# Optimization experiments

Hardware: AMD Instinct MI355X
Metric: run time of the kernel (lower is better)

## Reference

```python
import jax, jax.numpy as jnp
import numpy as np

N = 50000   # nodes
E = 640000  # edges
IN = 128    # input feature dim (== H*C so every layer has a residual)
H = 4       # heads
C = 32      # out channels per head
L = 3       # layers
D = H * C   # 128, per-layer output width
NEG_SLOPE = 0.2
LN_EPS = 1e-5


def setup_inputs() -> dict:
    key = jax.random.key(0)
    ks = jax.random.split(key, 6)
    s = 0.1  # keep activations well-scaled
    x = jax.random.normal(ks[0], (N, IN), dtype=jnp.float32)
    edge_index = jax.random.randint(ks[1], (2, E), 0, N)
    Wl = jax.random.normal(ks[2], (L, IN, D), dtype=jnp.float32) * s
    bl = jnp.zeros((L, D), dtype=jnp.float32)
    Wr = jax.random.normal(ks[3], (L, IN, D), dtype=jnp.float32) * s
    br = jnp.zeros((L, D), dtype=jnp.float32)
    att = jax.random.normal(ks[4], (L, H, C), dtype=jnp.float32) * s
    bias = jnp.zeros((L, D), dtype=jnp.float32)
    gamma = jnp.ones((L, D), dtype=jnp.float32)
    beta = jnp.zeros((L, D), dtype=jnp.float32)
    return {"x": x, "edge_index": edge_index, "Wl": Wl, "bl": bl,
            "Wr": Wr, "br": br, "att": att, "bias": bias,
            "gamma": gamma, "beta": beta}


def _gatv2_layer(x, src, dst, Wl, bl, Wr, br, att, bias):
    # GATv2Conv (concat heads, eval mode so attention dropout is identity)
    xl = (x @ Wl + bl).reshape(N, H, C)  # source transform
    xr = (x @ Wr + br).reshape(N, H, C)  # target transform
    # edge-wise gather: message along edge j->i uses xl[j] + xr[i]
    e = jax.nn.leaky_relu(xl[src] + xr[dst], NEG_SLOPE)      # [E,H,C]
    logit = jnp.einsum('ehc,hc->eh', e, att)                  # [E,H]
    # segment softmax over incoming edges of each target node
    m = jax.ops.segment_max(logit, dst, num_segments=N)       # [N,H]
    a = jnp.exp(logit - m[dst])
    denom = jax.ops.segment_sum(a, dst, num_segments=N)       # [N,H]
    a = a / (denom[dst] + 1e-16)
    # scatter-aggregate weighted source messages
    out = jax.ops.segment_sum(a[:, :, None] * xl[src], dst, num_segments=N)
    return out.reshape(N, D) + bias


def _layer_norm(h, g, b):
    mu = jnp.mean(h, axis=-1, keepdims=True)
    var = jnp.mean((h - mu) ** 2, axis=-1, keepdims=True)
    return (h - mu) * jax.lax.rsqrt(var + LN_EPS) * g + b


def reference(x, edge_index, Wl, bl, Wr, br, att, bias, gamma, beta):
    src, dst = edge_index[0], edge_index[1]
    out = x
    for l in range(L):  # small fixed layer count
        h = jax.nn.relu(_gatv2_layer(out, src, dst, Wl[l], bl[l], Wr[l], br[l], att[l], bias[l]))
        h = _layer_norm(h, gamma[l], beta[l])
        out = h + out  # in_dim == hidden*heads, so residual at every layer
    return out
```

## Files before the change

kernel.cpp:

```cpp
#include <hip/hip_runtime.h>
#include <hip/hip_bf16.h>
#include <math.h>

#define N_NODES 50000
#define N_EDGES 640000
#define DIM 128
#define NLAYER 3
#define LN_EPS 1e-5f
#define LOG2E 1.44269504088896f
#define NSCAN 49

#if __has_builtin(__builtin_amdgcn_exp2f)
#define EXP2(x) __builtin_amdgcn_exp2f(x)
#else
#define EXP2(x) exp2f(x)
#endif

typedef __attribute__((ext_vector_type(8))) short bf16x8;
typedef __attribute__((ext_vector_type(4))) float f32x4;

__device__ inline ushort f2b(float f) {
    __hip_bfloat16 h = __float2bfloat16(f);
    return *reinterpret_cast<ushort*>(&h);
}
__device__ inline float bf_lo(unsigned u) { return __uint_as_float(u << 16); }
__device__ inline float bf_hi(unsigned u) { return __uint_as_float(u & 0xffff0000u); }
__device__ inline float lr(float t) { return fmaf(0.4f, fabsf(t), 0.6f * t); }
__device__ inline unsigned pack2(float a, float b) {
    return (unsigned)f2b(a) | ((unsigned)f2b(b) << 16);
}
__device__ inline int cw_of(int w) { return (w & 15) + 32 * (w >> 4); }

template<int CTRL>
__device__ inline float dppadd(float v) {
    int m = __builtin_amdgcn_update_dpp(0, __float_as_int(v), CTRL, 0xF, 0xF, true);
    return v + __int_as_float(m);
}
__device__ inline float reduce16(float v) {
    v = dppadd<0x124>(v);
    v = dppadd<0x128>(v);
    v = dppadd<0xB1>(v);
    v = dppadd<0x4E>(v);
    return v;
}


__global__ __launch_bounds__(256) void fusedinit(
    const float* __restrict__ x, unsigned* __restrict__ curb,
    const float* __restrict__ Wl, const float* __restrict__ Wr, ushort* __restrict__ Wt,
    const int* __restrict__ dst, int* __restrict__ deg,
    const float* __restrict__ att, const float* __restrict__ bias,
    const float* __restrict__ gamma, const float* __restrict__ beta,
    float2* __restrict__ params)
{
    int b = blockIdx.x, t = threadIdx.x;
    if (b < 12500) {
        int i = b * 256 + t;
        int node = i >> 6, w = i & 63;
        int c = cw_of(w);
        curb[i] = pack2(x[node * DIM + c], x[node * DIM + c + 16]);
    } else if (b < 12884) {
        int i = (b - 12500) * 256 + t;
        if (i < NLAYER * 2 * DIM * DIM) {
            int p = i & 127, n = (i >> 7) & 127, mat = (i >> 14) & 1, l = i >> 15;
            int c = cw_of(p >> 1) + (p & 1) * 16;
            const float* W = mat ? Wr : Wl;
            Wt[i] = f2b(W[l * DIM * DIM + c * DIM + n]);
        }
    } else if (b < 15384) {
        int e = (b - 12884) * 256 + t;
        atomicAdd(&deg[dst[e]], 1);
    } else {
        int i = t;
        if (i < NLAYER * 64) {
            int l = i >> 6, w = i & 63;
            int c = cw_of(w);
            const float* A = att + l * DIM;
            const float* B = bias + l * DIM;
            const float* G = gamma + l * DIM;
            const float* E = beta + l * DIM;
            params[l * 256 + w]       = make_float2(A[c] * LOG2E, A[c + 16] * LOG2E);
            params[l * 256 + 64 + w]  = make_float2(B[c], B[c + 16]);
            params[l * 256 + 128 + w] = make_float2(G[c], G[c + 16]);
            params[l * 256 + 192 + w] = make_float2(E[c], E[c + 16]);
        }
    }
}


__global__ __launch_bounds__(1024) void scan1(const int* __restrict__ deg,
                                              int* __restrict__ rowptr,
                                              int* __restrict__ bsum,
                                              int* __restrict__ blockhist) {
    __shared__ int sd[1024];
    __shared__ int lh[256];
    int t = threadIdx.x;
    int idx = blockIdx.x * 1024 + t;
    if (t < 256) lh[t] = 0;
    __syncthreads();
    int v = (idx < N_NODES) ? deg[idx] : 0;
    if (idx < N_NODES) atomicAdd(&lh[v < 255 ? v : 255], 1);
    sd[t] = v;
    __syncthreads();
    for (int off = 1; off < 1024; off <<= 1) {
        int add = (t >= off) ? sd[t - off] : 0;
        __syncthreads();
        sd[t] += add;
        __syncthreads();
    }
    if (idx < N_NODES) rowptr[idx + 1] = sd[t];
    if (t == 1023) bsum[blockIdx.x] = sd[1023];
    if (t < 256) blockhist[blockIdx.x * 256 + t] = lh[t];
}

__global__ __launch_bounds__(1024) void midscan(const int* __restrict__ bsum,
                                                int* __restrict__ bcarry,
                                                const int* __restrict__ blockhist,
                                                int* __restrict__ bboff) {
    __shared__ int sh[256];
    int t = threadIdx.x;
    if (t < 256) {
        int tot = 0;
        for (int b = 0; b < NSCAN; ++b) tot += blockhist[b * 256 + t];
        sh[t] = tot;
    }
    __syncthreads();
    for (int off = 1; off < 256; off <<= 1) {
        int add = 0;
        if (t < 256 && t >= off) add = sh[t - off];
        __syncthreads();
        if (t < 256) sh[t] += add;
        __syncthreads();
    }
    if (t < 256) {
        int run = sh[255] - sh[t];
        for (int b = 0; b < NSCAN; ++b) {
            bboff[b * 256 + t] = run;
            run += blockhist[b * 256 + t];
        }
    }
    if (t == 0) {
        int c = 0;
        for (int b = 0; b < NSCAN; ++b) { bcarry[b] = c; c += bsum[b]; }
    }
}

__global__ __launch_bounds__(1024) void scan2(int* __restrict__ rowptr,
                                              const int* __restrict__ bcarry,
                                              const int* __restrict__ deg,
                                              const int* __restrict__ bboff,
                                              int* __restrict__ order) {
    __shared__ int lh[256];
    int t = threadIdx.x;
    int idx = blockIdx.x * 1024 + t;
    if (t < 256) lh[t] = 0;
    __syncthreads();
    int carry = bcarry[blockIdx.x];
    if (idx == 0) rowptr[0] = 0;
    if (idx < N_NODES) {
        rowptr[idx + 1] += carry;
        int d = deg[idx];
        int bin = d < 255 ? d : 255;
        int rank = atomicAdd(&lh[bin], 1);
        order[bboff[blockIdx.x * 256 + bin] + rank] = idx;
    }
}

__global__ void scatter_kernel(const int* __restrict__ src, const int* __restrict__ dst,
                               const int* __restrict__ rowptr, int* __restrict__ cnt,
                               int* __restrict__ esrc) {
    int e = blockIdx.x * blockDim.x + threadIdx.x;
    if (e < N_EDGES) {
        int d = dst[e];
        int pos = rowptr[d] + atomicAdd(&cnt[d], 1);
        esrc[pos] = src[e] << 8;
    }
}


__global__ __launch_bounds__(256) void gemm_mfma(
    const ushort* __restrict__ A,
    const ushort* __restrict__ Wt_l,
    const float* __restrict__ bl, const float* __restrict__ br,
    unsigned* __restrict__ xlb, unsigned* __restrict__ xrb)
{
    int mat = blockIdx.y;
    int rowbase = blockIdx.x * 128;
    int wid = threadIdx.x >> 6;
    int lane = threadIdx.x & 63;
    int wr = wid >> 1, wc = wid & 1;
    int m0 = rowbase + wr * 64, n0 = wc * 64;

    const ushort* W = Wt_l + mat * DIM * DIM;
    const float* bias = mat ? br : bl;
    unsigned* out = mat ? xrb : xlb;

    int fr = lane & 15;
    int kg = lane >> 4;

    bf16x8 af[4][4], bfr[4][4];
    #pragma unroll
    for (int mf = 0; mf < 4; ++mf) {
        int row = m0 + mf * 16 + fr;
        if (row > N_NODES - 1) row = N_NODES - 1;
        const ushort* p = A + (size_t)row * DIM + kg * 8;
        #pragma unroll
        for (int kf = 0; kf < 4; ++kf)
            af[mf][kf] = *reinterpret_cast<const bf16x8*>(p + kf * 32);
    }
    #pragma unroll
    for (int nf = 0; nf < 4; ++nf) {
        const ushort* p = W + (size_t)(n0 + nf * 16 + fr) * DIM + kg * 8;
        #pragma unroll
        for (int kf = 0; kf < 4; ++kf)
            bfr[nf][kf] = *reinterpret_cast<const bf16x8*>(p + kf * 32);
    }

    f32x4 acc[4][4];
    #pragma unroll
    for (int mf = 0; mf < 4; ++mf)
        #pragma unroll
        for (int nf = 0; nf < 4; ++nf)
            acc[mf][nf] = (f32x4){0.f, 0.f, 0.f, 0.f};

    #pragma unroll
    for (int kf = 0; kf < 4; ++kf)
        #pragma unroll
        for (int mf = 0; mf < 4; ++mf)
            #pragma unroll
            for (int nf = 0; nf < 4; ++nf)
                acc[mf][nf] = __builtin_amdgcn_mfma_f32_16x16x32_bf16(
                    af[mf][kf], bfr[nf][kf], acc[mf][nf], 0, 0, 0);

    int col = lane & 15;
    int r4 = lane >> 4;
    float bb[4];
    #pragma unroll
    for (int nf = 0; nf < 4; ++nf) bb[nf] = bias[n0 + nf * 16 + col];

    #pragma unroll
    for (int mf = 0; mf < 4; ++mf) {
        #pragma unroll
        for (int pj = 0; pj < 2; ++pj) {
            int w = col + 32 * wc + 16 * pj;
            #pragma unroll
            for (int r = 0; r < 4; ++r) {
                int row = m0 + mf * 16 + r4 * 4 + r;
                if (row < N_NODES)
                    out[(size_t)row * 64 + w] =
                        pack2(acc[mf][2 * pj][r] + bb[2 * pj],
                              acc[mf][2 * pj + 1][r] + bb[2 * pj + 1]);
            }
        }
    }
}


template<int U>
__device__ inline void edge_batch(const char* __restrict__ xb,
                                  const int* __restrict__ esrc, int e, int laneoff,
                                  float ax, float ay, float xrx, float xry,
                                  float& s, float& ox, float& oy) {
    int j[U]; unsigned u[U]; float vx[U], vy[U], p[U];
    #pragma unroll
    for (int i = 0; i < U; ++i) j[i] = esrc[e + i];
    #pragma unroll
    for (int i = 0; i < U; ++i)
        u[i] = *(const unsigned*)(xb + j[i] + laneoff);
    #pragma unroll
    for (int i = 0; i < U; ++i) {
        vx[i] = bf_lo(u[i]); vy[i] = bf_hi(u[i]);
        p[i] = lr(vx[i] + xrx) * ax + lr(vy[i] + xry) * ay;
    }
    #pragma unroll
    for (int i = 0; i < U; ++i) p[i] = reduce16(p[i]);
    #pragma unroll
    for (int i = 0; i < U; ++i) {
        float w = EXP2(p[i]);
        s += w; ox = fmaf(w, vx[i], ox); oy = fmaf(w, vy[i], oy);
    }
}

__global__ __launch_bounds__(256) void agg_kernel(
    const unsigned* __restrict__ xlb2, const unsigned* __restrict__ xrb2,
    const int* __restrict__ esrc, const int* __restrict__ rowptr,
    const int* __restrict__ order, const float2* __restrict__ P4,
    unsigned* __restrict__ curb, float* __restrict__ outf, int last)
{
    int slot = blockIdx.x * 4 + (threadIdx.x >> 6);
    int lane = threadIdx.x & 63;
    if (slot >= N_NODES) return;
    int node = __builtin_amdgcn_readfirstlane(order[slot]);

    unsigned xru = xrb2[node * 64 + lane];
    float xrx = bf_lo(xru), xry = bf_hi(xru);
    float2 att2 = P4[lane];

    const char* xb = (const char*)xlb2;
    int laneoff = lane << 2;

    float s = 0.f, ox = 0.f, oy = 0.f;
    int e0 = rowptr[node], e1 = rowptr[node + 1];

    int e = e0;
    for (; e + 8 <= e1; e += 8)
        edge_batch<8>(xb, esrc, e, laneoff, att2.x, att2.y, xrx, xry, s, ox, oy);
    if (e + 4 <= e1) {
        edge_batch<4>(xb, esrc, e, laneoff, att2.x, att2.y, xrx, xry, s, ox, oy);
        e += 4;
    }
    for (; e < e1; ++e)
        edge_batch<1>(xb, esrc, e, laneoff, att2.x, att2.y, xrx, xry, s, ox, oy);

    float inv = 1.f / (s + 1e-16f);
    float2 b2 = P4[64 + lane];
    float gx = fmaxf(fmaf(ox, inv, b2.x), 0.f);
    float gy = fmaxf(fmaf(oy, inv, b2.y), 0.f);

    float sum = gx + gy;
    sum = reduce16(sum);
    sum += __shfl_xor(sum, 16);
    sum += __shfl_xor(sum, 32);
    float mu = sum * (1.f / 128.f);
    float dx = gx - mu, dy = gy - mu;
    float ss = dx * dx + dy * dy;
    ss = reduce16(ss);
    ss += __shfl_xor(ss, 16);
    ss += __shfl_xor(ss, 32);
    float rstd = rsqrtf(ss * (1.f / 128.f) + LN_EPS);

    float2 g2  = P4[128 + lane];
    float2 be2 = P4[192 + lane];
    unsigned old = curb[node * 64 + lane];
    float yx = fmaf(dx * rstd, g2.x, be2.x) + bf_lo(old);
    float yy = fmaf(dy * rstd, g2.y, be2.y) + bf_hi(old);

    if (last) {
        int c = cw_of(lane);
        outf[node * DIM + c] = yx;
        outf[node * DIM + c + 16] = yy;
    } else {
        curb[node * 64 + lane] = pack2(yx, yy);
    }
}


extern "C" void kernel_launch(void* const* d_in, const int* in_sizes, int n_in,
                              void* d_out, int out_size, void* d_ws, size_t ws_size,
                              hipStream_t stream) {
    const float* x     = (const float*)d_in[0];
    const int*   ei    = (const int*)d_in[1];
    const float* Wl    = (const float*)d_in[2];
    const float* bl    = (const float*)d_in[3];
    const float* Wr    = (const float*)d_in[4];
    const float* br    = (const float*)d_in[5];
    const float* att   = (const float*)d_in[6];
    const float* bias  = (const float*)d_in[7];
    const float* gamma = (const float*)d_in[8];
    const float* beta  = (const float*)d_in[9];
    float* outf = (float*)d_out;

    char* ws = (char*)d_ws;
    size_t off = 0;
    auto alloc = [&](size_t bytes) -> void* {
        void* p = ws + off;
        off += (bytes + 255) & ~size_t(255);
        return p;
    };
    unsigned* curb = (unsigned*)alloc((size_t)N_NODES * 64 * 4);
    unsigned* xlb  = (unsigned*)alloc((size_t)N_NODES * 64 * 4);
    unsigned* xrb  = (unsigned*)alloc((size_t)N_NODES * 64 * 4);
    ushort* Wt     = (ushort*)alloc((size_t)NLAYER * 2 * DIM * DIM * 2);
    int* esrc      = (int*)alloc((size_t)N_EDGES * 4);
    int* rowptr    = (int*)alloc((size_t)(N_NODES + 1) * 4);
    int* zbase     = (int*)alloc((size_t)(2 * N_NODES + 2 * 64) * 4);
    int* deg = zbase, *cnt = zbase + N_NODES;
    int* bsum = cnt + N_NODES, *bcarry = bsum + 64;
    int* blockhist = (int*)alloc((size_t)NSCAN * 256 * 4);
    int* bboff     = (int*)alloc((size_t)NSCAN * 256 * 4);
    int* order     = (int*)alloc((size_t)N_NODES * 4);
    float2* params = (float2*)alloc((size_t)NLAYER * 256 * sizeof(float2));

    const int* srcArr = ei;
    const int* dstArr = ei + N_EDGES;

    hipMemsetAsync(zbase, 0, (size_t)(2 * N_NODES + 2 * 64) * 4, stream);
    fusedinit<<<15385, 256, 0, stream>>>(x, curb, Wl, Wr, Wt, dstArr, deg,
                                         att, bias, gamma, beta, params);
    scan1<<<NSCAN, 1024, 0, stream>>>(deg, rowptr, bsum, blockhist);
    midscan<<<1, 1024, 0, stream>>>(bsum, bcarry, blockhist, bboff);
    scan2<<<NSCAN, 1024, 0, stream>>>(rowptr, bcarry, deg, bboff, order);
    scatter_kernel<<<(N_EDGES + 255) / 256, 256, 0, stream>>>(srcArr, dstArr, rowptr, cnt, esrc);

    for (int l = 0; l < NLAYER; ++l) {
        gemm_mfma<<<dim3((N_NODES + 127) / 128, 2), 256, 0, stream>>>(
            (const ushort*)curb, Wt + (size_t)l * 2 * DIM * DIM,
            bl + (size_t)l * DIM, br + (size_t)l * DIM, xlb, xrb);
        agg_kernel<<<(N_NODES + 3) / 4, 256, 0, stream>>>(
            xlb, xrb, esrc, rowptr, order, params + (size_t)l * 256,
            curb, outf, l == NLAYER - 1 ? 1 : 0);
    }
}
```

Measured before the change: 261.5 us.

## Software-pipeline edge gathers in aggregation and replace memset with zero kernel

The aggregation loop now prefetches the next batch of eight source indices and feature gathers while computing the current batch, using a double-buffered register scheme. The tail is handled by a masked eight-wide gather with clamped indices instead of separate 4- and 1-wide paths. The aim is to hide gather latency behind the attention math. It also replaces hipMemsetAsync with a small zero-fill kernel to cut launch overhead. The extra in-flight registers may lower occupancy.

```diff
diff --git a/kernel.cpp b/kernel.cpp
--- a/kernel.cpp
+++ b/kernel.cpp
@@ -42,6 +42,12 @@
     v = dppadd<0xB1>(v);
     v = dppadd<0x4E>(v);
     return v;
+}
+
+
+__global__ __launch_bounds__(256) void zerofill(int4* __restrict__ p, int n4) {
+    int i = blockIdx.x * 256 + threadIdx.x;
+    if (i < n4) p[i] = make_int4(0, 0, 0, 0);
 }
 
 
@@ -256,28 +262,38 @@
 }
 
 
-template<int U>
-__device__ inline void edge_batch(const char* __restrict__ xb,
-                                  const int* __restrict__ esrc, int e, int laneoff,
-                                  float ax, float ay, float xrx, float xry,
-                                  float& s, float& ox, float& oy) {
-    int j[U]; unsigned u[U]; float vx[U], vy[U], p[U];
-    #pragma unroll
-    for (int i = 0; i < U; ++i) j[i] = esrc[e + i];
-    #pragma unroll
-    for (int i = 0; i < U; ++i)
+__device__ inline void gather8(const char* __restrict__ xb, int laneoff,
+                               const int j[8], unsigned u[8]) {
+    #pragma unroll
+    for (int i = 0; i < 8; ++i)
         u[i] = *(const unsigned*)(xb + j[i] + laneoff);
-    #pragma unroll
-    for (int i = 0; i < U; ++i) {
-        vx[i] = bf_lo(u[i]); vy[i] = bf_hi(u[i]);
-        p[i] = lr(vx[i] + xrx) * ax + lr(vy[i] + xry) * ay;
-    }
-    #pragma unroll
-    for (int i = 0; i < U; ++i) p[i] = reduce16(p[i]);
-    #pragma unroll
-    for (int i = 0; i < U; ++i) {
-        float w = EXP2(p[i]);
-        s += w; ox = fmaf(w, vx[i], ox); oy = fmaf(w, vy[i], oy);
+}
+
+__device__ inline void compute8(const unsigned u[8], float ax, float ay,
+                                float xrx, float xry,
+                                float& s, float& ox, float& oy) {
+    #pragma unroll
+    for (int i = 0; i < 8; ++i) {
+        float vx = bf_lo(u[i]), vy = bf_hi(u[i]);
+        float p = lr(vx + xrx) * ax + lr(vy + xry) * ay;
+        p = reduce16(p);
+        float w = EXP2(p);
+        s += w; ox = fmaf(w, vx, ox); oy = fmaf(w, vy, oy);
+    }
+}
+
+__device__ inline void computeT(const unsigned u[8], float ax, float ay,
+                                float xrx, float xry,
+                                float& s, float& ox, float& oy, int rem) {
+    #pragma unroll
+    for (int i = 0; i < 8; ++i) {
+        if (i < rem) {
+            float vx = bf_lo(u[i]), vy = bf_hi(u[i]);
+            float p = lr(vx + xrx) * ax + lr(vy + xry) * ay;
+            p = reduce16(p);
+            float w = EXP2(p);
+            s += w; ox = fmaf(w, vx, ox); oy = fmaf(w, vy, oy);
+        }
     }
 }
 
@@ -301,16 +317,47 @@
 
     float s = 0.f, ox = 0.f, oy = 0.f;
     int e0 = rowptr[node], e1 = rowptr[node + 1];
-
-    int e = e0;
-    for (; e + 8 <= e1; e += 8)
-        edge_batch<8>(xb, esrc, e, laneoff, att2.x, att2.y, xrx, xry, s, ox, oy);
-    if (e + 4 <= e1) {
-        edge_batch<4>(xb, esrc, e, laneoff, att2.x, att2.y, xrx, xry, s, ox, oy);
-        e += 4;
-    }
-    for (; e < e1; ++e)
-        edge_batch<1>(xb, esrc, e, laneoff, att2.x, att2.y, xrx, xry, s, ox, oy);
+    int nb = (e1 - e0) >> 3;
+    int rem = (e1 - e0) & 7;
+
+    int jc[8], jn[8];
+    unsigned uc[8], un[8];
+
+    if (nb > 0) {
+        #pragma unroll
+        for (int i = 0; i < 8; ++i) jc[i] = esrc[e0 + i];
+        gather8(xb, laneoff, jc, uc);
+    }
+    int ec = e0;
+    for (int b = 1; b < nb; ++b) {
+        int en = ec + 8;
+        #pragma unroll
+        for (int i = 0; i < 8; ++i) jn[i] = esrc[en + i];
+        gather8(xb, laneoff, jn, un);
+        compute8(uc, att2.x, att2.y, xrx, xry, s, ox, oy);
+        #pragma unroll
+        for (int i = 0; i < 8; ++i) uc[i] = un[i];
+        ec = en;
+    }
+    if (nb > 0) {
+        if (rem) {
+            int et = ec + 8;
+            #pragma unroll
+            for (int i = 0; i < 8; ++i)
+                jn[i] = esrc[et + (i < rem ? i : rem - 1)];
+            gather8(xb, laneoff, jn, un);
+            compute8(uc, att2.x, att2.y, xrx, xry, s, ox, oy);
+            computeT(un, att2.x, att2.y, xrx, xry, s, ox, oy, rem);
+        } else {
+            compute8(uc, att2.x, att2.y, xrx, xry, s, ox, oy);
+        }
+    } else if (rem) {
+        #pragma unroll
+        for (int i = 0; i < 8; ++i)
+            jc[i] = esrc[e0 + (i < rem ? i : rem - 1)];
+        gather8(xb, laneoff, jc, uc);
+        computeT(uc, att2.x, att2.y, xrx, xry, s, ox, oy, rem);
+    }
 
     float inv = 1.f / (s + 1e-16f);
     float2 b2 = P4[64 + lane];
@@ -384,7 +431,8 @@
     const int* srcArr = ei;
     const int* dstArr = ei + N_EDGES;
 
-    hipMemsetAsync(zbase, 0, (size_t)(2 * N_NODES + 2 * 64) * 4, stream);
+    int n4 = (2 * N_NODES + 2 * 64) / 4;
+    zerofill<<<(n4 + 255) / 256, 256, 0, stream>>>((int4*)zbase, n4);
     fusedinit<<<15385, 256, 0, stream>>>(x, curb, Wl, Wr, Wt, dstArr, deg,
                                          att, bias, gamma, beta, params);
     scan1<<<NSCAN, 1024, 0, stream>>>(deg, rowptr, bsum, blockhist);
```

Measured after the change: 257.7 us. About the same (-1.5%).

## Split aggregation per head with head-major layout and padded 4-edge CSR rows

Applied to the files above, without the earlier changes.

Stores xl/xr head-major, so each head's 32 channels sit in a contiguous 64-byte row. Aggregation is split into a per-head kernel, where each wave handles one head of one node and processes four edges at once (16 lanes each) from 4-aligned padded CSR rows, plus a separate LayerNorm/residual kernel. The goal is smaller gathered rows, better cache locality per head, and more edge-level parallelism. In exchange it adds an extra kernel, a bf16 round-trip for the aggregated output, padding waste on short rows, and a custom zero-fill kernel in place of memset.

```diff
diff --git a/kernel.cpp b/kernel.cpp
--- a/kernel.cpp
+++ b/kernel.cpp
@@ -4,6 +4,7 @@
 
 #define N_NODES 50000
 #define N_EDGES 640000
+#define EPAD (N_EDGES + 4 * N_NODES)
 #define DIM 128
 #define NLAYER 3
 #define LN_EPS 1e-5f
@@ -42,6 +43,12 @@
     v = dppadd<0xB1>(v);
     v = dppadd<0x4E>(v);
     return v;
+}
+
+
+__global__ __launch_bounds__(256) void zerofill(int4* __restrict__ p, int n4) {
+    int i = blockIdx.x * 256 + threadIdx.x;
+    if (i < n4) p[i] = make_int4(0, 0, 0, 0);
 }
 
 
@@ -100,7 +107,7 @@
     __syncthreads();
     int v = (idx < N_NODES) ? deg[idx] : 0;
     if (idx < N_NODES) atomicAdd(&lh[v < 255 ? v : 255], 1);
-    sd[t] = v;
+    sd[t] = (v + 3) & ~3;
     __syncthreads();
     for (int off = 1; off < 1024; off <<= 1) {
         int add = (t >= off) ? sd[t - off] : 0;
@@ -173,7 +180,7 @@
     if (e < N_EDGES) {
         int d = dst[e];
         int pos = rowptr[d] + atomicAdd(&cnt[d], 1);
-        esrc[pos] = src[e] << 8;
+        esrc[pos] = src[e] << 6;
     }
 }
 
@@ -182,7 +189,7 @@
     const ushort* __restrict__ A,
     const ushort* __restrict__ Wt_l,
     const float* __restrict__ bl, const float* __restrict__ br,
-    unsigned* __restrict__ xlb, unsigned* __restrict__ xrb)
+    unsigned* __restrict__ xlh, unsigned* __restrict__ xrh)
 {
     int mat = blockIdx.y;
     int rowbase = blockIdx.x * 128;
@@ -193,7 +200,7 @@
 
     const ushort* W = Wt_l + mat * DIM * DIM;
     const float* bias = mat ? br : bl;
-    unsigned* out = mat ? xrb : xlb;
+    unsigned* out = mat ? xrh : xlh;
 
     int fr = lane & 15;
     int kg = lane >> 4;
@@ -242,12 +249,12 @@
     for (int mf = 0; mf < 4; ++mf) {
         #pragma unroll
         for (int pj = 0; pj < 2; ++pj) {
-            int w = col + 32 * wc + 16 * pj;
+            int h = 2 * wc + pj;
             #pragma unroll
             for (int r = 0; r < 4; ++r) {
                 int row = m0 + mf * 16 + r4 * 4 + r;
                 if (row < N_NODES)
-                    out[(size_t)row * 64 + w] =
+                    out[((size_t)(h * N_NODES + row) << 4) + col] =
                         pack2(acc[mf][2 * pj][r] + bb[2 * pj],
                               acc[mf][2 * pj + 1][r] + bb[2 * pj + 1]);
             }
@@ -256,66 +263,66 @@
 }
 
 
-template<int U>
-__device__ inline void edge_batch(const char* __restrict__ xb,
-                                  const int* __restrict__ esrc, int e, int laneoff,
-                                  float ax, float ay, float xrx, float xry,
-                                  float& s, float& ox, float& oy) {
-    int j[U]; unsigned u[U]; float vx[U], vy[U], p[U];
-    #pragma unroll
-    for (int i = 0; i < U; ++i) j[i] = esrc[e + i];
-    #pragma unroll
-    for (int i = 0; i < U; ++i)
-        u[i] = *(const unsigned*)(xb + j[i] + laneoff);
-    #pragma unroll
-    for (int i = 0; i < U; ++i) {
-        vx[i] = bf_lo(u[i]); vy[i] = bf_hi(u[i]);
-        p[i] = lr(vx[i] + xrx) * ax + lr(vy[i] + xry) * ay;
-    }
-    #pragma unroll
-    for (int i = 0; i < U; ++i) p[i] = reduce16(p[i]);
-    #pragma unroll
-    for (int i = 0; i < U; ++i) {
-        float w = EXP2(p[i]);
-        s += w; ox = fmaf(w, vx[i], ox); oy = fmaf(w, vy[i], oy);
-    }
-}
-
-__global__ __launch_bounds__(256) void agg_kernel(
-    const unsigned* __restrict__ xlb2, const unsigned* __restrict__ xrb2,
-    const int* __restrict__ esrc, const int* __restrict__ rowptr,
-    const int* __restrict__ order, const float2* __restrict__ P4,
+__global__ __launch_bounds__(256) void agg_head(
+    const unsigned* __restrict__ xlh, const unsigned* __restrict__ xrh,
+    const int* __restrict__ esrc, const int* __restrict__ prow,
+    const int* __restrict__ deg, const int* __restrict__ order,
+    const float2* __restrict__ P4, unsigned* __restrict__ aggh)
+{
+    int bid = blockIdx.x;
+    int h = bid & 3;
+    int slot = ((bid >> 2) << 2) + (threadIdx.x >> 6);
+    int lane = threadIdx.x & 63;
+    int ww = lane & 15;
+    int q  = lane >> 4;
+    int node = __builtin_amdgcn_readfirstlane(order[slot]);
+
+    float2 att2 = P4[(h << 4) | ww];
+    unsigned xru = xrh[((size_t)(h * N_NODES + node) << 4) + ww];
+    float xrx = bf_lo(xru), xry = bf_hi(xru);
+    const char* xb = (const char*)xlh + (size_t)h * N_NODES * 64;
+    int laneoff = ww << 2;
+
+    float s = 0.f, ox = 0.f, oy = 0.f;
+    int e0 = prow[node];
+    int dt = deg[node];
+    int nit = (dt + 3) >> 2;
+
+    #pragma unroll 2
+    for (int it = 0; it < nit; ++it) {
+        int e = e0 + it * 4;
+        int4 jj = *reinterpret_cast<const int4*>(esrc + e);
+        int j = q == 0 ? jj.x : q == 1 ? jj.y : q == 2 ? jj.z : jj.w;
+        unsigned u = *(const unsigned*)(xb + j + laneoff);
+        float vx = bf_lo(u), vy = bf_hi(u);
+        float p = fmaf(lr(vy + xry), att2.y, lr(vx + xrx) * att2.x);
+        p = reduce16(p);
+        int rem = dt - it * 4;
+        float w = (q < rem) ? EXP2(p) : 0.f;
+        s += w; ox = fmaf(w, vx, ox); oy = fmaf(w, vy, oy);
+    }
+    s  += __shfl_xor(s, 16);  s  += __shfl_xor(s, 32);
+    ox += __shfl_xor(ox, 16); ox += __shfl_xor(ox, 32);
+    oy += __shfl_xor(oy, 16); oy += __shfl_xor(oy, 32);
+    float inv = 1.f / (s + 1e-16f);
+    if (lane < 16)
+        aggh[((size_t)(h * N_NODES + node) << 4) + ww] = pack2(ox * inv, oy * inv);
+}
+
+
+__global__ __launch_bounds__(256) void ln_res(
+    const unsigned* __restrict__ aggh, const float2* __restrict__ P4,
     unsigned* __restrict__ curb, float* __restrict__ outf, int last)
 {
-    int slot = blockIdx.x * 4 + (threadIdx.x >> 6);
+    int node = blockIdx.x * 4 + (threadIdx.x >> 6);
     int lane = threadIdx.x & 63;
-    if (slot >= N_NODES) return;
-    int node = __builtin_amdgcn_readfirstlane(order[slot]);
-
-    unsigned xru = xrb2[node * 64 + lane];
-    float xrx = bf_lo(xru), xry = bf_hi(xru);
-    float2 att2 = P4[lane];
-
-    const char* xb = (const char*)xlb2;
-    int laneoff = lane << 2;
-
-    float s = 0.f, ox = 0.f, oy = 0.f;
-    int e0 = rowptr[node], e1 = rowptr[node + 1];
-
-    int e = e0;
-    for (; e + 8 <= e1; e += 8)
-        edge_batch<8>(xb, esrc, e, laneoff, att2.x, att2.y, xrx, xry, s, ox, oy);
-    if (e + 4 <= e1) {
-        edge_batch<4>(xb, esrc, e, laneoff, att2.x, att2.y, xrx, xry, s, ox, oy);
-        e += 4;
-    }
-    for (; e < e1; ++e)
-        edge_batch<1>(xb, esrc, e, laneoff, att2.x, att2.y, xrx, xry, s, ox, oy);
-
-    float inv = 1.f / (s + 1e-16f);
+    int h = lane >> 4, ww = lane & 15;
+    unsigned u = aggh[((size_t)(h * N_NODES + node) << 4) + ww];
+    float ox = bf_lo(u), oy = bf_hi(u);
+
     float2 b2 = P4[64 + lane];
-    float gx = fmaxf(fmaf(ox, inv, b2.x), 0.f);
-    float gy = fmaxf(fmaf(oy, inv, b2.y), 0.f);
+    float gx = fmaxf(ox + b2.x, 0.f);
+    float gy = fmaxf(oy + b2.y, 0.f);
 
     float sum = gx + gy;
     sum = reduce16(sum);
@@ -368,23 +375,28 @@
         return p;
     };
     unsigned* curb = (unsigned*)alloc((size_t)N_NODES * 64 * 4);
-    unsigned* xlb  = (unsigned*)alloc((size_t)N_NODES * 64 * 4);
-    unsigned* xrb  = (unsigned*)alloc((size_t)N_NODES * 64 * 4);
+    unsigned* xlh  = (unsigned*)alloc((size_t)4 * N_NODES * 16 * 4);
+    unsigned* xrh  = (unsigned*)alloc((size_t)4 * N_NODES * 16 * 4);
+    unsigned* aggh = (unsigned*)alloc((size_t)4 * N_NODES * 16 * 4);
     ushort* Wt     = (ushort*)alloc((size_t)NLAYER * 2 * DIM * DIM * 2);
-    int* esrc      = (int*)alloc((size_t)N_EDGES * 4);
-    int* rowptr    = (int*)alloc((size_t)(N_NODES + 1) * 4);
+    size_t zoff0 = off;
     int* zbase     = (int*)alloc((size_t)(2 * N_NODES + 2 * 64) * 4);
+    int* esrc      = (int*)alloc((size_t)EPAD * 4);
+    size_t zbytes = (ws + off) - (char*)zbase;
     int* deg = zbase, *cnt = zbase + N_NODES;
     int* bsum = cnt + N_NODES, *bcarry = bsum + 64;
+    int* rowptr    = (int*)alloc((size_t)(N_NODES + 1) * 4);
     int* blockhist = (int*)alloc((size_t)NSCAN * 256 * 4);
     int* bboff     = (int*)alloc((size_t)NSCAN * 256 * 4);
     int* order     = (int*)alloc((size_t)N_NODES * 4);
     float2* params = (float2*)alloc((size_t)NLAYER * 256 * sizeof(float2));
+    (void)zoff0;
 
     const int* srcArr = ei;
     const int* dstArr = ei + N_EDGES;
 
-    hipMemsetAsync(zbase, 0, (size_t)(2 * N_NODES + 2 * 64) * 4, stream);
+    int n4 = (int)(zbytes / 16);
+    zerofill<<<(n4 + 255) / 256, 256, 0, stream>>>((int4*)zbase, n4);
     fusedinit<<<15385, 256, 0, stream>>>(x, curb, Wl, Wr, Wt, dstArr, deg,
                                          att, bias, gamma, beta, params);
     scan1<<<NSCAN, 1024, 0, stream>>>(deg, rowptr, bsum, blockhist);
@@ -395,9 +407,10 @@
     for (int l = 0; l < NLAYER; ++l) {
         gemm_mfma<<<dim3((N_NODES + 127) / 128, 2), 256, 0, stream>>>(
             (const ushort*)curb, Wt + (size_t)l * 2 * DIM * DIM,
-            bl + (size_t)l * DIM, br + (size_t)l * DIM, xlb, xrb);
-        agg_kernel<<<(N_NODES + 3) / 4, 256, 0, stream>>>(
-            xlb, xrb, esrc, rowptr, order, params + (size_t)l * 256,
-            curb, outf, l == NLAYER - 1 ? 1 : 0);
-    }
-}
+            bl + (size_t)l * DIM, br + (size_t)l * DIM, xlh, xrh);
+        agg_head<<<50000, 256, 0, stream>>>(
+            xlh, xrh, esrc, rowptr, deg, order, params + (size_t)l * 256, aggh);
+        ln_res<<<12500, 256, 0, stream>>>(
+            aggh, params + (size_t)l * 256, curb, outf, l == NLAYER - 1 ? 1 : 0);
+    }
+}
```

Result: slower. 436.8 us (+67.0%).
